# Kernel tuning notes

Hardware: AMD Instinct MI355X
Metric: run time of the kernel (lower is better)

The kernel has to match this reference:

```python
import jax, jax.numpy as jnp
import numpy as np
import math
from jax import lax

N = 5          # kernel_size (hard-coded PHT assumes 5x5)
K = N // 2     # 2
EPS = 1e-6
THETA = 0.7

def _pht_kernel_np():
    # H_i = cos(2*pi*2*r^2 + 0*theta) on the 5x5 grid, times calibrated spectral weights, plus eps
    coords = np.arange(N, dtype=np.float32) - K
    gv, gu = np.meshgrid(coords, coords, indexing='ij')  # torch.meshgrid default is 'ij'
    r2 = (gu ** 2 + gv ** 2) / (K * K + EPS)
    H = np.cos(2.0 * math.pi * 2.0 * r2).astype(np.float32)
    target = np.zeros((N, N), np.float32)
    target[K, K] = -4.0
    target[K - 1, K] = 1.0
    target[K + 1, K] = 1.0
    target[K, K - 1] = 1.0
    target[K, K + 1] = 1.0
    sw = np.where(target != 0, target / H, 0.0).astype(np.float32)
    return (H * sw + EPS).astype(np.float32)  # (5,5)

def _rotation_maps_np():
    # Replicates rotate_kernel exactly: float32 cos/sin, int() truncation, later (h,w) overwrite.
    angles = np.linspace(0, 2 * np.pi, 8, endpoint=False)
    SH = np.zeros((8, N, N), np.int32)
    SW = np.zeros((8, N, N), np.int32)
    M = np.zeros((8, N, N), np.float32)
    for ai, a in enumerate(angles):
        c = float(np.cos(np.float32(a)))
        s = float(np.sin(np.float32(a)))
        for h in range(N):
            for w in range(N):
                rh = int(h * c + w * (-s))
                rw = int(h * s + w * c)
                if 0 <= rh < N and 0 <= rw < N:
                    SH[ai, rh, rw] = h
                    SW[ai, rh, rw] = w
                    M[ai, rh, rw] = 1.0
    return SH, SW, M

_PHT = jnp.asarray(_pht_kernel_np())                     # (5,5)
_sh, _sw, _m = _rotation_maps_np()
_SH = jnp.asarray(_sh)
_SW = jnp.asarray(_sw)
_MASK = jnp.asarray(_m)

def setup_inputs() -> dict:
    key = jax.random.key(0)
    k1, k2 = jax.random.split(key)
    x = jax.random.normal(k1, (32, 64, 128, 128), dtype=jnp.float32)
    weight = jax.random.normal(k2, (64, 64, 5, 5), dtype=jnp.float32) * 0.05
    alpha = jnp.ones((1,), dtype=jnp.float32)
    return {"x": x, "weight": weight, "alpha": alpha}

def reference(x, weight, alpha):
    # Branch 1: PHT-modulated weight, averaged over 8 SO(2) rotations.
    # pht_kernel is (C_in,1,5,5) with identical values per channel -> broadcast (5,5).
    w_eff = weight * alpha[0] * _PHT[None, None]          # (Co,Ci,5,5)
    # rotated[o,i,a,rh,rw] = w_eff[o,i,SH[a,rh,rw],SW[a,rh,rw]] * MASK
    rotated = w_eff[:, :, _SH, _SW] * _MASK               # (Co,Ci,8,5,5)
    # conv is linear in weight: mean of 8 convs == conv with mean kernel
    mean_k = rotated.mean(axis=2)                         # (Co,Ci,5,5)
    out = lax.conv_general_dilated(
        x, mean_k, window_strides=(1, 1), padding=[(2, 2), (2, 2)],
        dimension_numbers=("NCHW", "OIHW", "NCHW"))
    # Branch 2: 1x1 kernel_diff; rotation of a 1x1 kernel is identity, mean of 8 == single conv.
    kd = weight.sum(axis=(2, 3))                          # (Co,Ci)
    out_diff = jnp.einsum("oi,bihw->bohw", kd, x)
    return out - THETA * out_diff
```

## Files before the change

kernel.cpp:

```cpp
#include <hip/hip_runtime.h>
#include <stdint.h>

typedef __attribute__((ext_vector_type(8))) __bf16 bf16x8;
typedef __attribute__((ext_vector_type(16))) float f32x16;
typedef __attribute__((ext_vector_type(4))) unsigned int u32x4;
typedef __attribute__((ext_vector_type(4))) float f32x4;
typedef unsigned int u32;
typedef unsigned short u16;

#define THETA 0.7f

__host__ __device__ constexpr float pht_val(int q) {
  return (q == 12) ? (-4.0f + 1e-6f)
       : (q == 7 || q == 11 || q == 13 || q == 17) ? (1.0f + 1e-6f)
       : 1e-6f;
}

__device__ __forceinline__ u16 f2bf(float v) {
  u32 u = __builtin_bit_cast(u32, v);
  return (u16)((u + 0x7fffu + ((u >> 16) & 1u)) >> 16);
}

__global__ __launch_bounds__(256) void k_prep(const float* __restrict__ wgt,
                                              const float* __restrict__ alpha,
                                              u16* __restrict__ apack) {
  int t = blockIdx.x * 256 + threadIdx.x;
  int o = t >> 6, ci = t & 63;
  const float* wp = wgt + ((size_t)(o * 64 + ci)) * 25;
  float wv[25], sumw = 0.f;
#pragma unroll
  for (int p = 0; p < 25; ++p) { wv[p] = wp[p]; sumw += wv[p]; }
  float keff[25];
#pragma unroll
  for (int p = 0; p < 25; ++p) keff[p] = pht_val(p) * wv[p];
  constexpr int TP[33] = {0,1,2,3,4,6,7,9,12,13,  0,1,2,3,4,  0, 0, 0,
                          0,5,10,15,20,  0,5,6,10,11,12,15,17,20,21};
  constexpr int TQ[33] = {5,6,12,17,23,10,16,22,20,21,  0,5,10,15,20,  5, 0, 5,
                          0,6,7,8,9,  5,6,2,12,8,4,17,9,23,14};
#pragma unroll
  for (int e = 0; e < 33; ++e) keff[TP[e]] += pht_val(TQ[e]) * wv[TQ[e]];

  float al = alpha[0];
  int kc = ci >> 4, oh = o >> 5;
  int lane = ((ci >> 3) & 1) * 32 + (o & 31);
#pragma unroll
  for (int p = 0; p < 25; ++p) {
    float v = al * (keff[p] * 0.125f);
    if (p == 12) v -= THETA * sumw;
    size_t idx = ((((size_t)p * 4 + kc) * 2 + oh) * 64 + lane) * 8 + (ci & 7);
    apack[idx] = f2bf(v);
  }
}

__global__ __launch_bounds__(256) void k_xcast(const float* __restrict__ x,
                                               u16* __restrict__ xt) {
  __shared__ u16 lt[64][130];
  int bid = blockIdx.x;
  int n = bid >> 7, y = bid & 127;
  const float* xb = x + (size_t)n * 64 * 16384 + (size_t)y * 128;
  int t = threadIdx.x;
#pragma unroll
  for (int it = 0; it < 8; ++it) {
    int idx = it * 256 + t;
    int i = idx >> 5, p4 = (idx & 31) * 4;
    f32x4 v = *(const f32x4*)(xb + (size_t)i * 16384 + p4);
    lt[i][p4 + 0] = f2bf(v.x); lt[i][p4 + 1] = f2bf(v.y);
    lt[i][p4 + 2] = f2bf(v.z); lt[i][p4 + 3] = f2bf(v.w);
  }
  __syncthreads();
  u32* xtb = (u32*)(xt + (size_t)(n * 128 + y) * 8192);
#pragma unroll
  for (int it = 0; it < 16; ++it) {
    int idx = it * 256 + t;
    int px = idx >> 5, i2 = idx & 31;
    u32 w = (u32)lt[2 * i2][px] | ((u32)lt[2 * i2 + 1][px] << 16);
    xtb[(size_t)px * 32 + i2] = w;
  }
}

#define ROWB 9216

#define MM(A, B, C) __builtin_amdgcn_mfma_f32_32x32x16_bf16((A), __builtin_bit_cast(bf16x8, (B)), (C), 0, 0, 0)

#define LDBR(S, DX, KC) do {                                                \
    const char* pb_ = pcol + (DX) * 128;                                    \
    int gx_ = ((((KC) * 2 + lhi) ^ ((l31 + (DX)) & 7)) << 4);               \
    br##S##0 = *(const u32x4*)(pb_ + 0 * ROWB + gx_);                       \
    br##S##1 = *(const u32x4*)(pb_ + 1 * ROWB + gx_);                       \
    br##S##2 = *(const u32x4*)(pb_ + 2 * ROWB + gx_);                       \
    br##S##3 = *(const u32x4*)(pb_ + 3 * ROWB + gx_);                       \
    br##S##4 = *(const u32x4*)(pb_ + 4 * ROWB + gx_);                       \
    br##S##5 = *(const u32x4*)(pb_ + 5 * ROWB + gx_);                       \
    br##S##6 = *(const u32x4*)(pb_ + 6 * ROWB + gx_);                       \
    br##S##7 = *(const u32x4*)(pb_ + 7 * ROWB + gx_);                       \
  } while (0)

#define LDAF(S, DX, KC) do {                                                \
    af##S##0 = apb[(size_t)((0 * 5 + (DX)) * 512 + (KC) * 128)];            \
    af##S##1 = apb[(size_t)((1 * 5 + (DX)) * 512 + (KC) * 128)];            \
    af##S##2 = apb[(size_t)((2 * 5 + (DX)) * 512 + (KC) * 128)];            \
    af##S##3 = apb[(size_t)((3 * 5 + (DX)) * 512 + (KC) * 128)];            \
    af##S##4 = apb[(size_t)((4 * 5 + (DX)) * 512 + (KC) * 128)];            \
  } while (0)

#define BURST(S) do {                                                       \
    bf16x8 A_;                                                              \
    A_ = __builtin_bit_cast(bf16x8, af##S##0);                              \
    a0 = MM(A_, br##S##0, a0); a1 = MM(A_, br##S##1, a1);                   \
    a2 = MM(A_, br##S##2, a2); a3 = MM(A_, br##S##3, a3);                   \
    A_ = __builtin_bit_cast(bf16x8, af##S##1);                              \
    a0 = MM(A_, br##S##1, a0); a1 = MM(A_, br##S##2, a1);                   \
    a2 = MM(A_, br##S##3, a2); a3 = MM(A_, br##S##4, a3);                   \
    A_ = __builtin_bit_cast(bf16x8, af##S##2);                              \
    a0 = MM(A_, br##S##2, a0); a1 = MM(A_, br##S##3, a1);                   \
    a2 = MM(A_, br##S##4, a2); a3 = MM(A_, br##S##5, a3);                   \
    A_ = __builtin_bit_cast(bf16x8, af##S##3);                              \
    a0 = MM(A_, br##S##3, a0); a1 = MM(A_, br##S##4, a1);                   \
    a2 = MM(A_, br##S##5, a2); a3 = MM(A_, br##S##6, a3);                   \
    A_ = __builtin_bit_cast(bf16x8, af##S##4);                              \
    a0 = MM(A_, br##S##4, a0); a1 = MM(A_, br##S##5, a1);                   \
    a2 = MM(A_, br##S##6, a2); a3 = MM(A_, br##S##7, a3);                   \
  } while (0)

#define SGB __builtin_amdgcn_sched_group_barrier
#define SCHED_FULL() do {                                                   \
    SGB(0x020, 5, 0);                           \
    SGB(0x100, 2, 0); SGB(0x008, 5, 0);                                     \
    SGB(0x100, 2, 0); SGB(0x008, 5, 0);                                     \
    SGB(0x100, 2, 0); SGB(0x008, 5, 0);                                     \
    SGB(0x100, 2, 0); SGB(0x008, 5, 0);                                     \
  } while (0)

#define ITER(CUR, NXT, DXN, KCN) do {                                       \
    LDBR(NXT, DXN, KCN); LDAF(NXT, DXN, KCN); BURST(CUR); SCHED_FULL();     \
  } while (0)

__global__ __launch_bounds__(256, 2) void k_conv(const u16* __restrict__ xt,
                                                 const u32x4* __restrict__ apv,
                                                 float* __restrict__ out) {
  __shared__ char tile[8 * ROWB];
  int bid = blockIdx.x;
  int lg = (bid & 7) * 256 + (bid >> 3);
  int ph = lg & 1, yt = (lg >> 1) & 31, n = lg >> 6;
  int y0 = yt * 4, px0 = ph * 64;
  int tid = threadIdx.x;
  int l = tid & 63, wv = tid >> 6;

#pragma unroll
  for (int rr = 0; rr < 2; ++rr) {
    int r = 2 * wv + rr;
    int sy = y0 + r - 2;
    char* rowbase = tile + r * ROWB;
    if ((unsigned)sy < 128u) {
      const char* xrow = (const char*)xt + ((size_t)(n * 128 + sy) * 16384)
                         + (ptrdiff_t)(px0 - 2) * 128;
      int g = l & 7;
#pragma unroll
      for (int it = 0; it < 9; ++it) {
        int gi = it * 64 + l;
        int c = gi >> 3;
        bool valid = ((unsigned)(px0 + c - 2) < 128u) && (c < 68);
        if (valid) {
          const char* src = xrow + c * 128 + ((g ^ (c & 7)) << 4);
          __builtin_amdgcn_global_load_lds(
              (const __attribute__((address_space(1))) u32*)src,
              (__attribute__((address_space(3))) u32*)(rowbase + it * 1024),
              16, 0, 0);
        } else {
          u32x4 z = {0u, 0u, 0u, 0u};
          *(u32x4*)(rowbase + it * 1024 + l * 16) = z;
        }
      }
    } else {
      u32x4 z = {0u, 0u, 0u, 0u};
#pragma unroll
      for (int it = 0; it < 9; ++it)
        *(u32x4*)(rowbase + it * 1024 + l * 16) = z;
    }
  }

  int oh = wv >> 1, q32 = wv & 1;
  int l31 = l & 31, lhi = l >> 5;
  const u32x4* apb = apv + (size_t)(oh * 64 + l);
  const char* pcol = tile + (q32 * 32 + l31) * 128;

  u32x4 brA0, brA1, brA2, brA3, brA4, brA5, brA6, brA7;
  u32x4 brB0, brB1, brB2, brB3, brB4, brB5, brB6, brB7;
  u32x4 afA0, afA1, afA2, afA3, afA4;
  u32x4 afB0, afB1, afB2, afB3, afB4;

  LDAF(A, 0, 0);
  __syncthreads();
  LDBR(A, 0, 0);

  f32x16 a0 = 0, a1 = 0, a2 = 0, a3 = 0;

  ITER(A, B, 0, 1);
  ITER(B, A, 0, 2);
  ITER(A, B, 0, 3);
  ITER(B, A, 1, 0);
  ITER(A, B, 1, 1);
  ITER(B, A, 1, 2);
  ITER(A, B, 1, 3);
  ITER(B, A, 2, 0);
  ITER(A, B, 2, 1);
  ITER(B, A, 2, 2);
  ITER(A, B, 2, 3);
  ITER(B, A, 3, 0);
  ITER(A, B, 3, 1);
  ITER(B, A, 3, 2);
  ITER(A, B, 3, 3);
  ITER(B, A, 4, 0);
  ITER(A, B, 4, 1);
  ITER(B, A, 4, 2);
  ITER(A, B, 4, 3);
  BURST(B);

  float* ob = out + ((size_t)(n * 64 + oh * 32) * 128 + y0) * 128
              + px0 + q32 * 32 + l31;
#pragma unroll
  for (int rg = 0; rg < 16; ++rg) {
    int orow = (rg & 3) + 8 * (rg >> 2) + 4 * lhi;
    float* obr = ob + (size_t)orow * 16384;
    obr[0]   = a0[rg];
    obr[128] = a1[rg];
    obr[256] = a2[rg];
    obr[384] = a3[rg];
  }
}

extern "C" void kernel_launch(void* const* d_in, const int* in_sizes, int n_in,
                              void* d_out, int out_size, void* d_ws, size_t ws_size,
                              hipStream_t stream) {
  const float* x     = (const float*)d_in[0];
  const float* wgt   = (const float*)d_in[1];
  const float* alpha = (const float*)d_in[2];
  float* out = (float*)d_out;

  u16* apack = (u16*)d_ws;
  u16* xt    = (u16*)((char*)d_ws + (1 << 20));

  k_prep <<<16,   256, 0, stream>>>(wgt, alpha, apack);
  k_xcast<<<4096, 256, 0, stream>>>(x, xt);
  k_conv <<<2048, 256, 0, stream>>>(xt, (const u32x4*)apack, out);
}
```

Before: 140.5 us.

## Fuse fp32-to-bf16 input transpose into conv kernel tile load

Removes the separate k_xcast pass that converted x to a channel-interleaved bf16 buffer. The conv kernel now reads fp32 x directly, converts it to bf16, packs channel pairs and writes them into the swizzled LDS tile, including halo columns. This avoids writing and re-reading the intermediate buffer and saves a launch. In exchange, each block re-reads 8 input rows for 4 output rows (2x overlap in fp32), uses plain loads instead of async global_load_lds, and does conversion ALU work inside the conv kernel.

```diff
diff --git a/kernel.cpp b/kernel.cpp
--- a/kernel.cpp
+++ b/kernel.cpp
@@ -4,7 +4,7 @@
 typedef __attribute__((ext_vector_type(8))) __bf16 bf16x8;
 typedef __attribute__((ext_vector_type(16))) float f32x16;
 typedef __attribute__((ext_vector_type(4))) unsigned int u32x4;
-typedef __attribute__((ext_vector_type(4))) float f32x4;
+typedef __attribute__((ext_vector_type(2))) float f32x2;
 typedef unsigned int u32;
 typedef unsigned short u16;
 
@@ -49,32 +49,6 @@
     if (p == 12) v -= THETA * sumw;
     size_t idx = ((((size_t)p * 4 + kc) * 2 + oh) * 64 + lane) * 8 + (ci & 7);
     apack[idx] = f2bf(v);
-  }
-}
-
-__global__ __launch_bounds__(256) void k_xcast(const float* __restrict__ x,
-                                               u16* __restrict__ xt) {
-  __shared__ u16 lt[64][130];
-  int bid = blockIdx.x;
-  int n = bid >> 7, y = bid & 127;
-  const float* xb = x + (size_t)n * 64 * 16384 + (size_t)y * 128;
-  int t = threadIdx.x;
-#pragma unroll
-  for (int it = 0; it < 8; ++it) {
-    int idx = it * 256 + t;
-    int i = idx >> 5, p4 = (idx & 31) * 4;
-    f32x4 v = *(const f32x4*)(xb + (size_t)i * 16384 + p4);
-    lt[i][p4 + 0] = f2bf(v.x); lt[i][p4 + 1] = f2bf(v.y);
-    lt[i][p4 + 2] = f2bf(v.z); lt[i][p4 + 3] = f2bf(v.w);
-  }
-  __syncthreads();
-  u32* xtb = (u32*)(xt + (size_t)(n * 128 + y) * 8192);
-#pragma unroll
-  for (int it = 0; it < 16; ++it) {
-    int idx = it * 256 + t;
-    int px = idx >> 5, i2 = idx & 31;
-    u32 w = (u32)lt[2 * i2][px] | ((u32)lt[2 * i2 + 1][px] << 16);
-    xtb[(size_t)px * 32 + i2] = w;
   }
 }
 
@@ -135,7 +109,11 @@
     LDBR(NXT, DXN, KCN); LDAF(NXT, DXN, KCN); BURST(CUR); SCHED_FULL();     \
   } while (0)
 
-__global__ __launch_bounds__(256, 2) void k_conv(const u16* __restrict__ xt,
+#define TWR(RB, C, I2, W)                                                   \
+  *(u32*)((RB) + (C) * 128 + ((((I2) >> 2) ^ ((C) & 7)) << 4)               \
+          + (((I2) & 3) << 2)) = (W)
+
+__global__ __launch_bounds__(256, 2) void k_conv(const float* __restrict__ x,
                                                  const u32x4* __restrict__ apv,
                                                  float* __restrict__ out) {
   __shared__ char tile[8 * ROWB];
@@ -144,41 +122,54 @@
   int ph = lg & 1, yt = (lg >> 1) & 31, n = lg >> 6;
   int y0 = yt * 4, px0 = ph * 64;
   int tid = threadIdx.x;
-  int l = tid & 63, wv = tid >> 6;
-
-#pragma unroll
-  for (int rr = 0; rr < 2; ++rr) {
-    int r = 2 * wv + rr;
-    int sy = y0 + r - 2;
-    char* rowbase = tile + r * ROWB;
-    if ((unsigned)sy < 128u) {
-      const char* xrow = (const char*)xt + ((size_t)(n * 128 + sy) * 16384)
-                         + (ptrdiff_t)(px0 - 2) * 128;
-      int g = l & 7;
-#pragma unroll
-      for (int it = 0; it < 9; ++it) {
-        int gi = it * 64 + l;
-        int c = gi >> 3;
-        bool valid = ((unsigned)(px0 + c - 2) < 128u) && (c < 68);
-        if (valid) {
-          const char* src = xrow + c * 128 + ((g ^ (c & 7)) << 4);
-          __builtin_amdgcn_global_load_lds(
-              (const __attribute__((address_space(1))) u32*)src,
-              (__attribute__((address_space(3))) u32*)(rowbase + it * 1024),
-              16, 0, 0);
-        } else {
-          u32x4 z = {0u, 0u, 0u, 0u};
-          *(u32x4*)(rowbase + it * 1024 + l * 16) = z;
+  int l = tid & 63;
+
+  {
+    const float* xn = x + (size_t)n * 64 * 16384;
+    int p = tid & 31;
+    int i2g = tid >> 5;
+    bool hthr = (tid < 128) && !(tid & 2);
+    int hi2 = tid >> 2, hp = tid & 1;
+    int hpx = hp ? px0 + 64 : px0 - 2;
+    int hc = hp ? 66 : 0;
+    bool hvalid = (unsigned)hpx < 128u;
+#pragma unroll
+    for (int rr = 0; rr < 8; ++rr) {
+      int sy = y0 + rr - 2;
+      bool rowok = (unsigned)sy < 128u;
+      char* rowbase = tile + rr * ROWB;
+      const float* xr = xn + (size_t)sy * 128;
+#pragma unroll
+      for (int m = 0; m < 4; ++m) {
+        int i2 = i2g * 4 + m;
+        f32x2 va = {0.f, 0.f}, vb = {0.f, 0.f};
+        if (rowok) {
+          const float* pa = xr + (size_t)(2 * i2) * 16384 + px0 + 2 * p;
+          va = *(const f32x2*)pa;
+          vb = *(const f32x2*)(pa + 16384);
         }
+        u32 w0 = (u32)f2bf(va.x) | ((u32)f2bf(vb.x) << 16);
+        u32 w1 = (u32)f2bf(va.y) | ((u32)f2bf(vb.y) << 16);
+        int c0 = 2 * p + 2;
+        TWR(rowbase, c0, i2, w0);
+        TWR(rowbase, c0 + 1, i2, w1);
       }
-    } else {
-      u32x4 z = {0u, 0u, 0u, 0u};
-#pragma unroll
-      for (int it = 0; it < 9; ++it)
-        *(u32x4*)(rowbase + it * 1024 + l * 16) = z;
+      if (hthr) {
+        f32x2 va = {0.f, 0.f}, vb = {0.f, 0.f};
+        if (rowok && hvalid) {
+          const float* pa = xr + (size_t)(2 * hi2) * 16384 + hpx;
+          va = *(const f32x2*)pa;
+          vb = *(const f32x2*)(pa + 16384);
+        }
+        u32 w0 = (u32)f2bf(va.x) | ((u32)f2bf(vb.x) << 16);
+        u32 w1 = (u32)f2bf(va.y) | ((u32)f2bf(vb.y) << 16);
+        TWR(rowbase, hc, hi2, w0);
+        TWR(rowbase, hc + 1, hi2, w1);
+      }
     }
   }
 
+  int wv = tid >> 6;
   int oh = wv >> 1, q32 = wv & 1;
   int l31 = l & 31, lhi = l >> 5;
   const u32x4* apb = apv + (size_t)(oh * 64 + l);
@@ -238,9 +229,7 @@
   float* out = (float*)d_out;
 
   u16* apack = (u16*)d_ws;
-  u16* xt    = (u16*)((char*)d_ws + (1 << 20));
-
-  k_prep <<<16,   256, 0, stream>>>(wgt, alpha, apack);
-  k_xcast<<<4096, 256, 0, stream>>>(x, xt);
-  k_conv <<<2048, 256, 0, stream>>>(xt, (const u32x4*)apack, out);
-}
+
+  k_prep<<<16,   256, 0, stream>>>(wgt, alpha, apack);
+  k_conv<<<2048, 256, 0, stream>>>(x, (const u32x4*)apack, out);
+}
```

New measurement: 126.7 us. 9.9% less time.
